# Optimization experiments

Measured on AMD Instinct MI355X. Metric: run time of the kernel, lower is better.

Reference implementation:

```python
import jax, jax.numpy as jnp
import numpy as np

B, H, W, P = 64, 480, 640, 8192  # batch, height, width, pairs per image


def setup_inputs() -> dict:
    key = jax.random.key(0)
    k0, k1, k2, k3, k4, k5 = jax.random.split(key, 6)
    output = jax.random.normal(k0, (B, 1, H, W), dtype=jnp.float32)
    x_A = jax.random.randint(k1, (B, P), 0, H)
    y_A = jax.random.randint(k2, (B, P), 0, W)
    x_B = jax.random.randint(k3, (B, P), 0, H)
    y_B = jax.random.randint(k4, (B, P), 0, W)
    # ordinal relation in {-1, 0, 1, 2}; 2 = invalid pair (filtered out)
    raw = jax.random.randint(k5, (B, P), 0, 4)
    ordinal_relation = jnp.where(raw == 3, -1, raw)
    return {
        "output": output,
        "x_A": x_A,
        "y_A": y_A,
        "x_B": x_B,
        "y_B": y_B,
        "ordinal_relation": ordinal_relation,
    }


def reference(output, x_A, y_A, x_B, y_B, ordinal_relation):
    b, _, h, w = output.shape
    depth = output[:, 0].reshape(b, h * w)  # [B, H*W]
    # coordinate gather for both pixels of each pair (vectorized over batch)
    z_A = jnp.take_along_axis(depth, x_A * w + y_A, axis=1)  # [B, P]
    z_B = jnp.take_along_axis(depth, x_B * w + y_B, axis=1)  # [B, P]
    pred = z_A - z_B
    t = ordinal_relation.astype(pred.dtype)
    valid = ordinal_relation != 2
    m_log = valid & (ordinal_relation != 0)  # ranking (log) term pairs
    m_sq = valid & (ordinal_relation == 0)   # equal-depth (squared) term pairs
    # log(1 + exp(-t * pred)) == softplus(-t * pred), numerically stable
    log_term = jax.nn.softplus(-t * pred)
    n_log = jnp.sum(m_log, axis=1).astype(pred.dtype)
    n_sq = jnp.sum(m_sq, axis=1).astype(pred.dtype)
    log_loss = jnp.sum(jnp.where(m_log, log_term, 0.0), axis=1) / n_log
    sq_loss = jnp.sum(jnp.where(m_sq, pred * pred, 0.0), axis=1) / n_sq
    return jnp.mean(log_loss + sq_loss)
```

## Files before the change

kernel.cpp:

```cpp
#include <hip/hip_runtime.h>

#define BB 64
#define HH 480
#define WW 640
#define PP 8192
#define CHUNKS 16
#define TPB 256
#define GRID (BB * CHUNKS)

typedef int v2i __attribute__((ext_vector_type(2)));


__global__ __launch_bounds__(TPB) void rdl_partial(
    const float* __restrict__ depth,
    const int*  __restrict__ xA,
    const int*  __restrict__ yA,
    const int*  __restrict__ xB,
    const int*  __restrict__ yB,
    const int*  __restrict__ rel,
    float4*     __restrict__ ws)
{
    const int bid = blockIdx.x;
    const int b   = bid & (BB - 1);
    const int c   = bid >> 6;
    const int tid = threadIdx.x;
    const int pair0 = b * PP + c * (PP / CHUNKS) + tid * 2;

    const v2i xa2 = __builtin_nontemporal_load(reinterpret_cast<const v2i*>(xA  + pair0));
    const v2i ya2 = __builtin_nontemporal_load(reinterpret_cast<const v2i*>(yA  + pair0));
    const v2i xb2 = __builtin_nontemporal_load(reinterpret_cast<const v2i*>(xB  + pair0));
    const v2i yb2 = __builtin_nontemporal_load(reinterpret_cast<const v2i*>(yB  + pair0));
    const v2i rr2 = __builtin_nontemporal_load(reinterpret_cast<const v2i*>(rel + pair0));

    const int xas[2] = {xa2.x, xa2.y};
    const int yas[2] = {ya2.x, ya2.y};
    const int xbs[2] = {xb2.x, xb2.y};
    const int ybs[2] = {yb2.x, yb2.y};
    const int rs [2] = {rr2.x, rr2.y};

    const float* __restrict__ img = depth + (size_t)b * (HH * WW);

    float zA[2], zB[2];
#pragma unroll
    for (int k = 0; k < 2; ++k) {
        const bool valid = (rs[k] != 2);
        const int iA = valid ? (xas[k] * WW + yas[k]) : 0;
        const int iB = valid ? (xbs[k] * WW + ybs[k]) : 0;
        zA[k] = img[iA];
        zB[k] = img[iB];
    }

    float s_log = 0.f, s_sq = 0.f;
    int   n_log = 0,   n_sq = 0;
#pragma unroll
    for (int k = 0; k < 2; ++k) {
        const float pred = zA[k] - zB[k];
        const int r = rs[k];
        if (r != 2) {
            if (r == 0) {
                s_sq += pred * pred;
                n_sq++;
            } else {
                const float x = -(float)r * pred;
                s_log += fmaxf(x, 0.f) + log1pf(expf(-fabsf(x)));
                n_log++;
            }
        }
    }

#pragma unroll
    for (int off = 32; off > 0; off >>= 1) {
        s_log += __shfl_down(s_log, off);
        s_sq  += __shfl_down(s_sq,  off);
        n_log += __shfl_down(n_log, off);
        n_sq  += __shfl_down(n_sq,  off);
    }

    __shared__ float4 lds[TPB / 64];
    const int wave = tid >> 6;
    if ((tid & 63) == 0)
        lds[wave] = make_float4(s_log, s_sq, (float)n_log, (float)n_sq);
    __syncthreads();

    if (tid == 0) {
        float4 acc = lds[0];
#pragma unroll
        for (int wv = 1; wv < TPB / 64; ++wv) {
            acc.x += lds[wv].x;
            acc.y += lds[wv].y;
            acc.z += lds[wv].z;
            acc.w += lds[wv].w;
        }
        ws[bid] = acc;
    }
}

__global__ __launch_bounds__(TPB) void rdl_final(
    const float4* __restrict__ ws,
    float*        __restrict__ out)
{
    const int tid   = threadIdx.x;
    const int batch = tid >> 2;
    const int sub   = tid & 3;
    float sl = 0.f, ss = 0.f, nl = 0.f, ns = 0.f;
#pragma unroll
    for (int k = 0; k < CHUNKS / 4; ++k) {
        const int chunk = sub * (CHUNKS / 4) + k;
        const float4 v = ws[chunk * BB + batch];
        sl += v.x; ss += v.y; nl += v.z; ns += v.w;
    }
#pragma unroll
    for (int off = 1; off < 4; off <<= 1) {
        sl += __shfl_xor(sl, off);
        ss += __shfl_xor(ss, off);
        nl += __shfl_xor(nl, off);
        ns += __shfl_xor(ns, off);
    }
    __shared__ float lossArr[BB];
    if (sub == 0)
        lossArr[batch] = sl / nl + ss / ns;
    __syncthreads();
    if (tid < BB) {
        float loss = lossArr[tid];
#pragma unroll
        for (int off = 32; off > 0; off >>= 1)
            loss += __shfl_down(loss, off);
        if (tid == 0)
            out[0] = loss * (1.0f / (float)BB);
    }
}

extern "C" void kernel_launch(void* const* d_in, const int* in_sizes, int n_in,
                              void* d_out, int out_size, void* d_ws, size_t ws_size,
                              hipStream_t stream) {
    const float* depth = (const float*)d_in[0];
    const int*   xA    = (const int*)d_in[1];
    const int*   yA    = (const int*)d_in[2];
    const int*   xB    = (const int*)d_in[3];
    const int*   yB    = (const int*)d_in[4];
    const int*   rel   = (const int*)d_in[5];
    float*       out   = (float*)d_out;
    float4*      ws    = (float4*)d_ws;

    rdl_partial<<<GRID, TPB, 0, stream>>>(depth, xA, yA, xB, yB, rel, ws);
    rdl_final<<<1, TPB, 0, stream>>>(ws, out);
}
```

Measured before the change: 18.72 us.

## Fuse final reduction into partial kernel via last-block atomic counter

Merges the two launches into one kernel. Each block publishes its partial sums with atomic exchanges and increments a global counter, and the block that sees the last count performs the final cross-batch reduction, reading partials through atomic adds of zero. This removes the second kernel launch and its dependency gap. In exchange it adds device-scope atomics and a serial tail in a single block. It also relies on the counter never being reset, using a modulo so it works across repeated calls.

```diff
diff --git a/kernel.cpp b/kernel.cpp
--- a/kernel.cpp
+++ b/kernel.cpp
@@ -11,14 +11,16 @@
 typedef int v2i __attribute__((ext_vector_type(2)));
 
 
-__global__ __launch_bounds__(TPB) void rdl_partial(
+__global__ __launch_bounds__(TPB) void rdl_fused(
     const float* __restrict__ depth,
     const int*  __restrict__ xA,
     const int*  __restrict__ yA,
     const int*  __restrict__ xB,
     const int*  __restrict__ yB,
     const int*  __restrict__ rel,
-    float4*     __restrict__ ws)
+    float*        __restrict__ ws,
+    unsigned int* __restrict__ counter,
+    float*        __restrict__ out)
 {
     const int bid = blockIdx.x;
     const int b   = bid & (BB - 1);
@@ -82,6 +84,7 @@
         lds[wave] = make_float4(s_log, s_sq, (float)n_log, (float)n_sq);
     __syncthreads();
 
+    __shared__ int lastFlag;
     if (tid == 0) {
         float4 acc = lds[0];
 #pragma unroll
@@ -91,23 +94,28 @@
             acc.z += lds[wv].z;
             acc.w += lds[wv].w;
         }
-        ws[bid] = acc;
+        const float o0 = atomicExch(&ws[bid * 4 + 0], acc.x);
+        const float o1 = atomicExch(&ws[bid * 4 + 1], acc.y);
+        const float o2 = atomicExch(&ws[bid * 4 + 2], acc.z);
+        const float o3 = atomicExch(&ws[bid * 4 + 3], acc.w);
+        asm volatile("" :: "v"(o0), "v"(o1), "v"(o2), "v"(o3) : "memory");
+        const unsigned int old = atomicAdd(counter, 1u);
+        lastFlag = ((old & (GRID - 1)) == (GRID - 1));
     }
-}
+    __syncthreads();
+    if (!lastFlag) return;
 
-__global__ __launch_bounds__(TPB) void rdl_final(
-    const float4* __restrict__ ws,
-    float*        __restrict__ out)
-{
-    const int tid   = threadIdx.x;
     const int batch = tid >> 2;
     const int sub   = tid & 3;
     float sl = 0.f, ss = 0.f, nl = 0.f, ns = 0.f;
 #pragma unroll
     for (int k = 0; k < CHUNKS / 4; ++k) {
         const int chunk = sub * (CHUNKS / 4) + k;
-        const float4 v = ws[chunk * BB + batch];
-        sl += v.x; ss += v.y; nl += v.z; ns += v.w;
+        const int base  = (chunk * BB + batch) * 4;
+        sl += atomicAdd(&ws[base + 0], 0.0f);
+        ss += atomicAdd(&ws[base + 1], 0.0f);
+        nl += atomicAdd(&ws[base + 2], 0.0f);
+        ns += atomicAdd(&ws[base + 3], 0.0f);
     }
 #pragma unroll
     for (int off = 1; off < 4; off <<= 1) {
@@ -140,8 +148,8 @@
     const int*   yB    = (const int*)d_in[4];
     const int*   rel   = (const int*)d_in[5];
     float*       out   = (float*)d_out;
-    float4*      ws    = (float4*)d_ws;
+    float*       ws    = (float*)d_ws;
+    unsigned int* counter = (unsigned int*)(ws + GRID * 4);
 
-    rdl_partial<<<GRID, TPB, 0, stream>>>(depth, xA, yA, xB, yB, rel, ws);
-    rdl_final<<<1, TPB, 0, stream>>>(ws, out);
+    rdl_fused<<<GRID, TPB, 0, stream>>>(depth, xA, yA, xB, yB, rel, ws, counter, out);
 }
```

Result: slower. 26.58 us (+42.0%).
